# Kernel optimization log

Hardware: AMD Instinct MI355X
Metric: run time of the kernel (lower is better)

The kernel has to match this reference:

```python
import jax, jax.numpy as jnp
import numpy as np

D_MODEL = 1024
N_HEAD = 16
D_K = D_MODEL // N_HEAD
B, S = 2, 2048


def setup_inputs() -> dict:
    key = jax.random.key(0)
    ks = jax.random.split(key, 12)
    sc = 1.0 / np.sqrt(D_MODEL)
    return {
        "q": jax.random.normal(ks[0], (B, S, D_MODEL), jnp.float32),
        "k": jax.random.normal(ks[1], (B, S, D_MODEL), jnp.float32),
        "v": jax.random.normal(ks[2], (B, S, D_MODEL), jnp.float32),
        "mask": jax.random.randint(ks[3], (B, S, S), 0, 2, jnp.int32),
        # learned params (torch Linear convention: y = x @ W + b with W pre-transposed)
        "wq": jax.random.normal(ks[4], (D_MODEL, D_MODEL), jnp.float32) * sc,
        "bq": jax.random.normal(ks[5], (D_MODEL,), jnp.float32) * sc,
        "wk": jax.random.normal(ks[6], (D_MODEL, D_MODEL), jnp.float32) * sc,  # no bias
        "wv": jax.random.normal(ks[7], (D_MODEL, D_MODEL), jnp.float32) * sc,
        "bv": jax.random.normal(ks[8], (D_MODEL,), jnp.float32) * sc,
        "wf": jax.random.normal(ks[9], (D_MODEL, D_MODEL), jnp.float32) * sc,
        "bf": jax.random.normal(ks[10], (D_MODEL,), jnp.float32) * sc,
    }


def reference(q, k, v, mask, wq, bq, wk, wv, bv, wf, bf):
    bs = q.shape[0]
    temperature = jnp.asarray(D_K ** 0.5, q.dtype)
    # projections -> [b, h, s, d_k]
    qh = (q @ wq + bq).reshape(bs, -1, N_HEAD, D_K).transpose(0, 2, 1, 3)
    kh = (k @ wk).reshape(bs, -1, N_HEAD, D_K).transpose(0, 2, 1, 3)
    vh = (v @ wv + bv).reshape(bs, -1, N_HEAD, D_K).transpose(0, 2, 1, 3)
    # scores [b, h, sq, sk]
    attn = jnp.einsum("bhqd,bhkd->bhqk", qh, kh) / temperature
    m0 = (mask[:, None, :, :] == 0)  # mask==0 -> masked out, broadcast over heads
    attn = jnp.where(m0, -jnp.inf, attn)
    attn = jax.nn.softmax(attn, axis=-1)
    attn = jnp.where(m0, 0.0, attn)
    out = jnp.einsum("bhqk,bhkd->bhqd", attn, vh)
    out = out.transpose(0, 2, 1, 3).reshape(bs, -1, D_MODEL)
    return out @ wf + bf  # dropout is identity in eval mode
```

## Files before the change

kernel.cpp:

```cpp
#include <hip/hip_runtime.h>

#define D_MODEL 1024
#define NHEAD   16
#define DK      64
#define BATCH   2
#define SEQ     2048

typedef __attribute__((ext_vector_type(8))) short bf16x8;
typedef __attribute__((ext_vector_type(4))) short bf16x4;
typedef __attribute__((ext_vector_type(4))) float f32x4;
typedef __attribute__((ext_vector_type(2))) int i32x2;

#define QSCALE 0.18033688011f

__device__ __forceinline__ unsigned short f2b(float x) {
  unsigned u = __builtin_bit_cast(unsigned, x);
  u = (u + 0x7fffu + ((u >> 16) & 1u)) >> 16;
  return (unsigned short)u;
}
__device__ __forceinline__ unsigned short f2b_rhu(float x) {
  return (unsigned short)((__builtin_bit_cast(unsigned, x) + 0x8000u) >> 16);
}
__device__ __forceinline__ int pk2(float a, float b) {
  unsigned ua = __builtin_bit_cast(unsigned, a) + 0x8000u;
  unsigned ub = __builtin_bit_cast(unsigned, b) + 0x8000u;
  return (int)__builtin_amdgcn_perm(ub, ua, 0x07060302u);
}
__device__ __forceinline__ int pk2u(unsigned ua, unsigned ub) {
  return (int)__builtin_amdgcn_perm(ub + 0x8000u, ua + 0x8000u, 0x07060302u);
}

typedef const __attribute__((address_space(1))) void* gas_p;
typedef __attribute__((address_space(3))) void* las_p;
__device__ __forceinline__ void gll16(const void* g, void* l) {
  __builtin_amdgcn_global_load_lds((gas_p)g, (las_p)l, 16, 0, 0);
}

__device__ __forceinline__ f32x4 mfma16(bf16x4 a, bf16x4 b, f32x4 c) {
#if __has_builtin(__builtin_amdgcn_mfma_f32_16x16x16bf16_1k)
  return __builtin_amdgcn_mfma_f32_16x16x16bf16_1k(a, b, c, 0, 0, 0);
#else
  f32x4 d;
  asm("v_mfma_f32_16x16x16_bf16 %0, %1, %2, %3" : "=v"(d) : "v"(a), "v"(b), "v"(c));
  return d;
#endif
}

__global__ __launch_bounds__(256) void prep_kernel(
    const float* __restrict__ q, const float* __restrict__ k, const float* __restrict__ v,
    unsigned short* __restrict__ qb, unsigned short* __restrict__ kb,
    unsigned short* __restrict__ vb,
    const float* __restrict__ wq, const float* __restrict__ wk,
    const float* __restrict__ wv, const float* __restrict__ wf,
    unsigned short* __restrict__ wqt, unsigned short* __restrict__ wkt,
    unsigned short* __restrict__ wvt, unsigned short* __restrict__ wft,
    const int* __restrict__ mask, unsigned long long* __restrict__ mbits) {
  int bid = blockIdx.x, t = threadIdx.x;
  if (bid < 6144) {
    int by = bid >> 11, bx = bid & 2047;
    const float* src = by == 0 ? q : (by == 1 ? k : v);
    unsigned short* dst = by == 0 ? qb : (by == 1 ? kb : vb);
    size_t i = ((size_t)bx * 256 + t) * 8;
    float4 x0 = *(const float4*)&src[i];
    float4 x1 = *(const float4*)&src[i + 4];
    int4 w;
    w.x = pk2(x0.x, x0.y); w.y = pk2(x0.z, x0.w);
    w.z = pk2(x1.x, x1.y); w.w = pk2(x1.z, x1.w);
    *(int4*)&dst[i] = w;
  } else if (bid < 7168) {
    __shared__ float tile[64][65];
    int idx = bid - 6144;
    int bz = idx >> 8, by = (idx >> 4) & 15, bx = idx & 15;
    const float* w; unsigned short* wt;
    switch (bz) {
      case 0: w = wq; wt = wqt; break;
      case 1: w = wk; wt = wkt; break;
      case 2: w = wv; wt = wvt; break;
      default: w = wf; wt = wft; break;
    }
    int r0 = by * 64, c0 = bx * 64;
    for (int i = 0; i < 16; ++i) {
      int idx2 = t + i * 256; int r = idx2 >> 6, c = idx2 & 63;
      tile[r][c] = w[(size_t)(r0 + r) * D_MODEL + c0 + c];
    }
    __syncthreads();
    for (int i = 0; i < 16; ++i) {
      int idx2 = t + i * 256; int r = idx2 >> 6, c = idx2 & 63;
      wt[(size_t)(c0 + r) * D_MODEL + r0 + c] = f2b(tile[c][r]);
    }
  } else {
    int idx = bid - 7168;
    int lane = t & 63, wave = t >> 6;
    size_t base = ((size_t)idx * 4 + wave) * 256;
    unsigned long long b0 = __ballot(mask[base + lane] != 0);
    unsigned long long b1 = __ballot(mask[base + 64 + lane] != 0);
    unsigned long long b2 = __ballot(mask[base + 128 + lane] != 0);
    unsigned long long b3 = __ballot(mask[base + 192 + lane] != 0);
    if (lane == 0) {
      unsigned long long* p = &mbits[(size_t)idx * 16 + wave * 4];
      p[0] = b0; p[1] = b1; p[2] = b2; p[3] = b3;
    }
  }
}

__global__ __launch_bounds__(256) void gemm_qkv_kernel(
    const unsigned short* __restrict__ qb, const unsigned short* __restrict__ kb,
    const unsigned short* __restrict__ vb,
    const unsigned short* __restrict__ wqt, const unsigned short* __restrict__ wkt,
    const unsigned short* __restrict__ wvt,
    const float* __restrict__ bq, const float* __restrict__ bv,
    unsigned short* __restrict__ qh, unsigned short* __restrict__ kh,
    unsigned short* __restrict__ vt) {
  __shared__ unsigned short SB[16640];
  int bid = blockIdx.x;
  int xcd = bid & 7, slot = bid >> 3;
  int mi = slot & 3, zn = slot >> 2;
  int z = zn >> 3;
  int n0 = (zn & 7) * 128;
  int m0 = (mi * 8 + xcd) * 128;
  const unsigned short* A; const unsigned short* Bt;
  switch (z) {
    case 0:  A = qb; Bt = wqt; break;
    case 1:  A = kb; Bt = wkt; break;
    default: A = vb; Bt = wvt; break;
  }
  int t = threadIdx.x, lane = t & 63, wave = t >> 6;
  int l16 = lane & 15, quad = lane >> 4;
  int wm = (wave & 1) * 64, wn = (wave >> 1) * 64;
  f32x4 zero = {0.f, 0.f, 0.f, 0.f};
  f32x4 acc[4][4];
  for (int mt = 0; mt < 4; ++mt) for (int nt = 0; nt < 4; ++nt) acc[mt][nt] = zero;

  int drow = lane >> 2, dcol = (lane & 3) * 8;
  const unsigned short* asrc = A  + (size_t)(m0 + wave * 32 + drow) * D_MODEL + dcol;
  const unsigned short* bsrc = Bt + (size_t)(n0 + wave * 32 + drow) * D_MODEL + dcol;
  int dst = wave * 1024 + lane * 8;

#pragma unroll
  for (int g = 0; g < 2; ++g) {
    gll16(asrc + (size_t)(g * 16) * D_MODEL, &SB[dst + g * 512]);
    gll16(bsrc + (size_t)(g * 16) * D_MODEL, &SB[4096 + dst + g * 512]);
  }
  for (int it = 0; it < 32; ++it) {
    __syncthreads();
    if (it + 1 < 32) {
      int nb = ((it + 1) & 1) * 8192, kn = (it + 1) * 32;
#pragma unroll
      for (int g = 0; g < 2; ++g) {
        gll16(asrc + (size_t)(g * 16) * D_MODEL + kn, &SB[nb + dst + g * 512]);
        gll16(bsrc + (size_t)(g * 16) * D_MODEL + kn, &SB[nb + 4096 + dst + g * 512]);
      }
    }
    int cb = (it & 1) * 8192;
    bf16x8 a[4], b[4];
    for (int mt = 0; mt < 4; ++mt)
      a[mt] = *(const bf16x8*)&SB[cb + (wm + mt * 16 + l16) * 32 + quad * 8];
    for (int nt = 0; nt < 4; ++nt)
      b[nt] = *(const bf16x8*)&SB[cb + 4096 + (wn + nt * 16 + l16) * 32 + quad * 8];
    for (int mt = 0; mt < 4; ++mt)
      for (int nt = 0; nt < 4; ++nt)
        acc[mt][nt] = __builtin_amdgcn_mfma_f32_16x16x32_bf16(a[mt], b[nt], acc[mt][nt], 0, 0, 0);
  }

  if (z == 2) {
    __syncthreads();
#pragma unroll
    for (int nt = 0; nt < 4; ++nt) {
      int col = wn + nt * 16 + l16;
      float bb = bv[n0 + col];
      for (int mt = 0; mt < 4; ++mt)
        for (int r = 0; r < 4; ++r)
          SB[col * 130 + wm + mt * 16 + quad * 4 + r] = f2b_rhu(acc[mt][nt][r] + bb);
    }
    __syncthreads();
    int c = t >> 1, hf = t & 1;
    int colg = n0 + c, hh = colg >> 6, dd = colg & 63;
    int b_ = m0 >> 11, sbase = m0 & (SEQ - 1);
    unsigned short* dstp = vt + (((size_t)(b_ * NHEAD + hh)) * DK + dd) * SEQ + sbase + hf * 64;
#pragma unroll
    for (int j = 0; j < 8; ++j)
      *(int4*)(dstp + j * 8) = *(const int4*)&SB[c * 130 + hf * 64 + j * 8];
  } else {
    __syncthreads();
#pragma unroll
    for (int nt = 0; nt < 4; ++nt) {
      int lcol = wn + nt * 16 + l16;
      float bb = (z == 0) ? bq[n0 + lcol] : 0.f;
      for (int mt = 0; mt < 4; ++mt)
        for (int r = 0; r < 4; ++r) {
          float val = acc[mt][nt][r] + bb;
          if (z == 0) val *= QSCALE;
          SB[(wm + mt * 16 + quad * 4 + r) * 130 + lcol] = f2b_rhu(val);
        }
    }
    __syncthreads();
    unsigned short* outp = (z == 0) ? qh : kh;
    int b_ = m0 >> 11, sbase = m0 & (SEQ - 1);
    int h0 = n0 >> 6, c = t & 7;
#pragma unroll
    for (int pass = 0; pass < 8; ++pass) {
      int rp = pass * 32 + (t >> 3);
      int srow = rp >> 1, part = rp & 1;
      unsigned short* dstp = outp +
          (((size_t)(b_ * NHEAD + h0 + part)) * SEQ + sbase + srow) * DK + c * 8;
      *(int4*)dstp = *(const int4*)&SB[srow * 130 + part * 64 + c * 8];
    }
  }
}

__global__ __launch_bounds__(256) void gemm_out_kernel(
    const unsigned short* __restrict__ A, const unsigned short* __restrict__ Bt,
    const float* __restrict__ bias, float* __restrict__ out) {
  __shared__ unsigned short As[8192], Bs[8192];
  int bid = blockIdx.x;
  int xcd = bid & 7, slot = bid >> 3;
  int mi = slot & 7, n0 = (slot >> 3) * 64;
  int m0 = (mi * 8 + xcd) * 64;
  int t = threadIdx.x, lane = t & 63, wave = t >> 6;
  int l16 = lane & 15, quad = lane >> 4;
  int wm = (wave & 1) * 32, wn = (wave >> 1) * 32;
  f32x4 zero = {0.f, 0.f, 0.f, 0.f};
  f32x4 acc[2][2];
  for (int mt = 0; mt < 2; ++mt) for (int nt = 0; nt < 2; ++nt) acc[mt][nt] = zero;

  int drow = lane >> 2, dcol = (lane & 3) * 8;
  const unsigned short* asrc = A  + (size_t)(m0 + wave * 16 + drow) * D_MODEL + dcol;
  const unsigned short* bsrc = Bt + (size_t)(n0 + wave * 16 + drow) * D_MODEL + dcol;
  int dst = wave * 512 + lane * 8;

#pragma unroll
  for (int hf = 0; hf < 2; ++hf) {
    gll16(asrc + hf * 32, &As[dst + hf * 2048]);
    gll16(bsrc + hf * 32, &Bs[dst + hf * 2048]);
  }
  for (int it = 0; it < 16; ++it) {
    __syncthreads();
    if (it + 1 < 16) {
      int nb = ((it + 1) & 1) * 4096, kn = (it + 1) * 64;
#pragma unroll
      for (int hf = 0; hf < 2; ++hf) {
        gll16(asrc + kn + hf * 32, &As[nb + dst + hf * 2048]);
        gll16(bsrc + kn + hf * 32, &Bs[nb + dst + hf * 2048]);
      }
    }
    int cb = (it & 1) * 4096;
#pragma unroll
    for (int half = 0; half < 2; ++half) {
      bf16x8 a[2], b[2];
      for (int mt = 0; mt < 2; ++mt)
        a[mt] = *(const bf16x8*)&As[cb + half * 2048 + (wm + mt * 16 + l16) * 32 + quad * 8];
      for (int nt = 0; nt < 2; ++nt)
        b[nt] = *(const bf16x8*)&Bs[cb + half * 2048 + (wn + nt * 16 + l16) * 32 + quad * 8];
      for (int mt = 0; mt < 2; ++mt)
        for (int nt = 0; nt < 2; ++nt)
          acc[mt][nt] = __builtin_amdgcn_mfma_f32_16x16x32_bf16(a[mt], b[nt], acc[mt][nt], 0, 0, 0);
    }
  }
  for (int nt = 0; nt < 2; ++nt) {
    int col = n0 + wn + nt * 16 + l16;
    float bb = bias[col];
    for (int mt = 0; mt < 2; ++mt)
      for (int r = 0; r < 4; ++r) {
        int row = m0 + wm + mt * 16 + quad * 4 + r;
        out[(size_t)row * D_MODEL + col] = acc[mt][nt][r] + bb;
      }
  }
}

__global__ __launch_bounds__(512, 4) void attn_kernel(
    const unsigned short* __restrict__ qh, const unsigned short* __restrict__ kh,
    const unsigned short* __restrict__ vt, const unsigned long long* __restrict__ mbits,
    unsigned short* __restrict__ attb) {
  __shared__ unsigned short Ks[16384];
  __shared__ unsigned short Vs[16384];
  int bid = blockIdx.x;
  int xcd = bid & 7, slot = bid >> 3;
  int bh_ = 4 * xcd + (slot >> 4);
  int qt = slot & 15;
  int b = bh_ >> 4, h = bh_ & 15;
  int t = threadIdx.x, lane = t & 63, wave = t >> 6;
  int l16 = lane & 15, quad = lane >> 4;
  size_t bh = (size_t)b * NHEAD + h;

  const unsigned short* Kg = kh + bh * SEQ * DK;
  const unsigned short* Vg = vt + bh * DK * SEQ;
  const unsigned long long* mrow = mbits + (size_t)b * SEQ * (SEQ / 64);
  int qrowb = qt * 128 + wave * 16;

  bf16x8 qf[2];
  {
    const unsigned short* Qg = qh + (bh * SEQ + (size_t)(qrowb + l16)) * DK;
    qf[0] = *(const bf16x8*)&Qg[quad * 8];
    qf[1] = *(const bf16x8*)&Qg[32 + quad * 8];
  }

  int ksrow = t >> 3;
  int kschk = ((t & 7) ^ (ksrow & 7)) * 8;
  const unsigned short* ksrc = Kg + (size_t)ksrow * DK + kschk;
  int vsrow = t >> 4;
  int vschk = ((t & 15) ^ (vsrow & 15)) * 8;
  const unsigned short* vsrc = Vg + (size_t)vsrow * SEQ + vschk;
  int sdst = t * 8;

  int x7 = l16 & 7;
  int ka0 = l16 * 64 + ((quad ^ x7) * 8);
  int ka1 = l16 * 64 + (((4 + quad) ^ x7) * 8);
  int va[2][4];
#pragma unroll
  for (int sub = 0; sub < 2; ++sub)
#pragma unroll
    for (int nt = 0; nt < 4; ++nt)
      va[sub][nt] = l16 * 128 + (((sub * 8 + nt * 2 + (quad >> 1)) ^ l16) * 8)
                    + (quad & 1) * 4;

  size_t mi0 = (size_t)(qrowb + l16) * (SEQ / 64);

  bf16x4 ones4;
#pragma unroll
  for (int i = 0; i < 4; ++i) ones4[i] = (short)0x3F80;

  f32x4 zero = {0.f, 0.f, 0.f, 0.f};
  f32x4 accO[4], accRS = zero;
#pragma unroll
  for (int dt = 0; dt < 4; ++dt) accO[dt] = zero;

#pragma unroll
  for (int g = 0; g < 2; ++g) {
    gll16(ksrc + (size_t)(g * 64) * DK, &Ks[g * 4096 + sdst]);
    gll16(vsrc + (size_t)(g * 32) * SEQ, &Vs[g * 4096 + sdst]);
  }

  for (int tk = 0; tk < SEQ / 128; ++tk) {
    __syncthreads();
    if (tk + 1 < SEQ / 128) {
      int nb = ((tk + 1) & 1) * 8192;
      const unsigned short* kn = ksrc + (size_t)(tk + 1) * 128 * DK;
      const unsigned short* vn = vsrc + (tk + 1) * 128;
#pragma unroll
      for (int g = 0; g < 2; ++g) {
        gll16(kn + (size_t)(g * 64) * DK, &Ks[nb + g * 4096 + sdst]);
        gll16(vn + (size_t)(g * 32) * SEQ, &Vs[nb + g * 4096 + sdst]);
      }
    }
    unsigned long long mA0 = mrow[mi0 + 2 * tk];
    unsigned long long mA1 = mrow[mi0 + 2 * tk + 1];

    int cb = (tk & 1) * 8192;
#pragma unroll
    for (int sub = 0; sub < 2; ++sub) {
      int kb_ = cb + sub * 4096;
      f32x4 accS[4];
#pragma unroll
      for (int nt = 0; nt < 4; ++nt) accS[nt] = zero;
      __builtin_amdgcn_s_setprio(1);
#pragma unroll
      for (int step = 0; step < 2; ++step) {
        int ka = step ? ka1 : ka0;
#pragma unroll
        for (int nt = 0; nt < 4; ++nt) {
          bf16x8 kf = *(const bf16x8*)&Ks[kb_ + ka + nt * 1024];
          accS[nt] = __builtin_amdgcn_mfma_f32_16x16x32_bf16(kf, qf[step], accS[nt], 0, 0, 0);
        }
      }
      __builtin_amdgcn_s_setprio(0);

      unsigned long long mq = (sub ? mA1 : mA0) >> (quad * 4);
      unsigned mlo = (unsigned)mq, mhi = (unsigned)(mq >> 32);
      bf16x4 ap[4];
#pragma unroll
      for (int nt = 0; nt < 4; ++nt) {
        unsigned w = (nt < 2) ? mlo : mhi;
        unsigned pu[4];
#pragma unroll
        for (int r = 0; r < 4; ++r) {
          float pv = __builtin_amdgcn_exp2f(accS[nt][r]);
          int msk = ((int)(w << (31 - ((nt & 1) * 16 + r)))) >> 31;
          pu[r] = __builtin_bit_cast(unsigned, pv) & (unsigned)msk;
        }
        i32x2 wv;
        wv[0] = pk2u(pu[0], pu[1]);
        wv[1] = pk2u(pu[2], pu[3]);
        ap[nt] = __builtin_bit_cast(bf16x4, wv);
      }

      __builtin_amdgcn_s_setprio(1);
#pragma unroll
      for (int nt = 0; nt < 4; ++nt)
        accRS = mfma16(ap[nt], ones4, accRS);
#pragma unroll
      for (int nt = 0; nt < 4; ++nt) {
        int vb_ = cb + va[sub][nt];
#pragma unroll
        for (int dt = 0; dt < 4; ++dt) {
          bf16x4 vf = *(const bf16x4*)&Vs[vb_ + dt * 2048];
          accO[dt] = mfma16(ap[nt], vf, accO[dt]);
        }
      }
      __builtin_amdgcn_s_setprio(0);
    }
  }

#pragma unroll
  for (int r = 0; r < 4; ++r) {
    float sden = accRS[r];
    float inv = sden > 0.f ? 1.f / sden : 0.f;
    int row = qrowb + quad * 4 + r;
    size_t ob = ((size_t)b * SEQ + row) * D_MODEL + (size_t)h * DK;
    for (int dt = 0; dt < 4; ++dt)
      attb[ob + dt * 16 + l16] = f2b_rhu(accO[dt][r] * inv);
  }
}

extern "C" void kernel_launch(void* const* d_in, const int* in_sizes, int n_in,
                              void* d_out, int out_size, void* d_ws, size_t ws_size,
                              hipStream_t stream) {
  (void)in_sizes; (void)n_in; (void)out_size; (void)ws_size;
  const float* q    = (const float*)d_in[0];
  const float* k    = (const float*)d_in[1];
  const float* v    = (const float*)d_in[2];
  const int*   mask = (const int*)d_in[3];
  const float* wq   = (const float*)d_in[4];
  const float* bq   = (const float*)d_in[5];
  const float* wk   = (const float*)d_in[6];
  const float* wv   = (const float*)d_in[7];
  const float* bv   = (const float*)d_in[8];
  const float* wf   = (const float*)d_in[9];
  const float* bf   = (const float*)d_in[10];

  char* ws = (char*)d_ws;
  unsigned short* wft  = (unsigned short*)(ws + 0);
  unsigned short* wqt  = (unsigned short*)(ws + 2097152);
  unsigned short* wkt  = (unsigned short*)(ws + 4194304);
  unsigned short* wvt  = (unsigned short*)(ws + 6291456);
  unsigned short* attb = (unsigned short*)(ws + 2097152);
  unsigned short* qhp  = (unsigned short*)(ws + 10485760);
  unsigned short* khp  = (unsigned short*)(ws + 18874368);
  unsigned short* vtp  = (unsigned short*)(ws + 27262976);
  unsigned long long* mbits = (unsigned long long*)(ws + 35651584);
  unsigned short* vb   = (unsigned short*)(ws + 36700160);
  unsigned short* qb   = (unsigned short*)d_out;
  unsigned short* kb   = (unsigned short*)d_out + 4194304;

  hipLaunchKernelGGL(prep_kernel, dim3(15360), dim3(256), 0, stream,
                     q, k, v, qb, kb, vb,
                     wq, wk, wv, wf, wqt, wkt, wvt, wft, mask, mbits);
  hipLaunchKernelGGL(gemm_qkv_kernel, dim3(768), dim3(256), 0, stream,
                     qb, kb, vb, wqt, wkt, wvt, bq, bv, qhp, khp, vtp);
  hipLaunchKernelGGL(attn_kernel, dim3(512), dim3(512), 0, stream,
                     qhp, khp, vtp, mbits, attb);
  hipLaunchKernelGGL(gemm_out_kernel, dim3(1024), dim3(256), 0, stream,
                     attb, wft, bf, (float*)d_out);
}
```

Baseline: 250.1 us.

## Switch attention kernel to 32x32x16 MFMA tiles with 4 waves per block

Rewrites the attention inner loop to use 32x32x16 bf16 MFMA instead of 16x16 variants, so each wave now handles 32 query rows. Blocks shrink from 512 to 256 threads. The V-transpose stage in the QKV GEMM permutes row order so the V layout in shared memory matches the new P-fragment layout. The aim is fewer MFMA issues and fewer LDS reads per unit of work, at the cost of more accumulator registers and fewer waves for latency hiding.

```diff
diff --git a/kernel.cpp b/kernel.cpp
--- a/kernel.cpp
+++ b/kernel.cpp
@@ -7,9 +7,9 @@
 #define SEQ     2048
 
 typedef __attribute__((ext_vector_type(8))) short bf16x8;
-typedef __attribute__((ext_vector_type(4))) short bf16x4;
 typedef __attribute__((ext_vector_type(4))) float f32x4;
-typedef __attribute__((ext_vector_type(2))) int i32x2;
+typedef __attribute__((ext_vector_type(16))) float f32x16;
+typedef __attribute__((ext_vector_type(4))) int i32x4;
 
 #define QSCALE 0.18033688011f
 
@@ -36,14 +36,8 @@
   __builtin_amdgcn_global_load_lds((gas_p)g, (las_p)l, 16, 0, 0);
 }
 
-__device__ __forceinline__ f32x4 mfma16(bf16x4 a, bf16x4 b, f32x4 c) {
-#if __has_builtin(__builtin_amdgcn_mfma_f32_16x16x16bf16_1k)
-  return __builtin_amdgcn_mfma_f32_16x16x16bf16_1k(a, b, c, 0, 0, 0);
-#else
-  f32x4 d;
-  asm("v_mfma_f32_16x16x16_bf16 %0, %1, %2, %3" : "=v"(d) : "v"(a), "v"(b), "v"(c));
-  return d;
-#endif
+__device__ __forceinline__ f32x16 mfma32(bf16x8 a, bf16x8 b, f32x16 c) {
+  return __builtin_amdgcn_mfma_f32_32x32x16_bf16(a, b, c, 0, 0, 0);
 }
 
 __global__ __launch_bounds__(256) void prep_kernel(
@@ -164,13 +158,14 @@
 
   if (z == 2) {
     __syncthreads();
+    int qs = ((quad & 1) << 1) | (quad >> 1);
 #pragma unroll
     for (int nt = 0; nt < 4; ++nt) {
       int col = wn + nt * 16 + l16;
       float bb = bv[n0 + col];
       for (int mt = 0; mt < 4; ++mt)
         for (int r = 0; r < 4; ++r)
-          SB[col * 130 + wm + mt * 16 + quad * 4 + r] = f2b_rhu(acc[mt][nt][r] + bb);
+          SB[col * 130 + wm + mt * 16 + qs * 4 + r] = f2b_rhu(acc[mt][nt][r] + bb);
     }
     __syncthreads();
     int c = t >> 1, hf = t & 1;
@@ -267,7 +262,7 @@
   }
 }
 
-__global__ __launch_bounds__(512, 4) void attn_kernel(
+__global__ __launch_bounds__(256, 2) void attn_kernel(
     const unsigned short* __restrict__ qh, const unsigned short* __restrict__ kh,
     const unsigned short* __restrict__ vt, const unsigned long long* __restrict__ mbits,
     unsigned short* __restrict__ attb) {
@@ -279,19 +274,20 @@
   int qt = slot & 15;
   int b = bh_ >> 4, h = bh_ & 15;
   int t = threadIdx.x, lane = t & 63, wave = t >> 6;
-  int l16 = lane & 15, quad = lane >> 4;
+  int l32 = lane & 31, hi = lane >> 5;
   size_t bh = (size_t)b * NHEAD + h;
 
   const unsigned short* Kg = kh + bh * SEQ * DK;
   const unsigned short* Vg = vt + bh * DK * SEQ;
   const unsigned long long* mrow = mbits + (size_t)b * SEQ * (SEQ / 64);
-  int qrowb = qt * 128 + wave * 16;
-
-  bf16x8 qf[2];
+  int qrowb = qt * 128 + wave * 32;
+
+  bf16x8 qf[4];
   {
-    const unsigned short* Qg = qh + (bh * SEQ + (size_t)(qrowb + l16)) * DK;
-    qf[0] = *(const bf16x8*)&Qg[quad * 8];
-    qf[1] = *(const bf16x8*)&Qg[32 + quad * 8];
+    const unsigned short* Qg = qh + (bh * SEQ + (size_t)(qrowb + l32)) * DK;
+#pragma unroll
+    for (int step = 0; step < 4; ++step)
+      qf[step] = *(const bf16x8*)&Qg[(step * 2 + hi) * 8];
   }
 
   int ksrow = t >> 3;
@@ -302,32 +298,28 @@
   const unsigned short* vsrc = Vg + (size_t)vsrow * SEQ + vschk;
   int sdst = t * 8;
 
-  int x7 = l16 & 7;
-  int ka0 = l16 * 64 + ((quad ^ x7) * 8);
-  int ka1 = l16 * 64 + (((4 + quad) ^ x7) * 8);
-  int va[2][4];
-#pragma unroll
-  for (int sub = 0; sub < 2; ++sub)
-#pragma unroll
-    for (int nt = 0; nt < 4; ++nt)
-      va[sub][nt] = l16 * 128 + (((sub * 8 + nt * 2 + (quad >> 1)) ^ l16) * 8)
-                    + (quad & 1) * 4;
-
-  size_t mi0 = (size_t)(qrowb + l16) * (SEQ / 64);
-
-  bf16x4 ones4;
-#pragma unroll
-  for (int i = 0; i < 4; ++i) ones4[i] = (short)0x3F80;
-
-  f32x4 zero = {0.f, 0.f, 0.f, 0.f};
-  f32x4 accO[4], accRS = zero;
-#pragma unroll
-  for (int dt = 0; dt < 4; ++dt) accO[dt] = zero;
-
-#pragma unroll
-  for (int g = 0; g < 2; ++g) {
-    gll16(ksrc + (size_t)(g * 64) * DK, &Ks[g * 4096 + sdst]);
-    gll16(vsrc + (size_t)(g * 32) * SEQ, &Vs[g * 4096 + sdst]);
+  int kx = l32 & 7;
+  int kaddr[4];
+#pragma unroll
+  for (int step = 0; step < 4; ++step)
+    kaddr[step] = l32 * 64 + (((step * 2 + hi) ^ kx) * 8);
+  int vx = l32 & 15;
+
+  size_t mi0 = (size_t)(qrowb + l32) * (SEQ / 64);
+
+  bf16x8 ones8;
+#pragma unroll
+  for (int i = 0; i < 8; ++i) ones8[i] = (short)0x3F80;
+
+  f32x16 zero16;
+#pragma unroll
+  for (int i = 0; i < 16; ++i) zero16[i] = 0.f;
+  f32x16 accO0 = zero16, accO1 = zero16, accRS = zero16;
+
+#pragma unroll
+  for (int g = 0; g < 4; ++g) {
+    gll16(ksrc + (size_t)(g * 32) * DK, &Ks[g * 2048 + sdst]);
+    gll16(vsrc + (size_t)(g * 16) * SEQ, &Vs[g * 2048 + sdst]);
   }
 
   for (int tk = 0; tk < SEQ / 128; ++tk) {
@@ -337,77 +329,71 @@
       const unsigned short* kn = ksrc + (size_t)(tk + 1) * 128 * DK;
       const unsigned short* vn = vsrc + (tk + 1) * 128;
 #pragma unroll
-      for (int g = 0; g < 2; ++g) {
-        gll16(kn + (size_t)(g * 64) * DK, &Ks[nb + g * 4096 + sdst]);
-        gll16(vn + (size_t)(g * 32) * SEQ, &Vs[nb + g * 4096 + sdst]);
-      }
-    }
-    unsigned long long mA0 = mrow[mi0 + 2 * tk];
-    unsigned long long mA1 = mrow[mi0 + 2 * tk + 1];
+      for (int g = 0; g < 4; ++g) {
+        gll16(kn + (size_t)(g * 32) * DK, &Ks[nb + g * 2048 + sdst]);
+        gll16(vn + (size_t)(g * 16) * SEQ, &Vs[nb + g * 2048 + sdst]);
+      }
+    }
+    unsigned long long m0 = mrow[mi0 + 2 * tk];
+    unsigned long long m1 = mrow[mi0 + 2 * tk + 1];
 
     int cb = (tk & 1) * 8192;
 #pragma unroll
-    for (int sub = 0; sub < 2; ++sub) {
-      int kb_ = cb + sub * 4096;
-      f32x4 accS[4];
-#pragma unroll
-      for (int nt = 0; nt < 4; ++nt) accS[nt] = zero;
+    for (int kt = 0; kt < 4; ++kt) {
+      f32x16 accS = zero16;
       __builtin_amdgcn_s_setprio(1);
 #pragma unroll
-      for (int step = 0; step < 2; ++step) {
-        int ka = step ? ka1 : ka0;
-#pragma unroll
-        for (int nt = 0; nt < 4; ++nt) {
-          bf16x8 kf = *(const bf16x8*)&Ks[kb_ + ka + nt * 1024];
-          accS[nt] = __builtin_amdgcn_mfma_f32_16x16x32_bf16(kf, qf[step], accS[nt], 0, 0, 0);
-        }
+      for (int step = 0; step < 4; ++step) {
+        bf16x8 kf = *(const bf16x8*)&Ks[cb + kt * 2048 + kaddr[step]];
+        accS = mfma32(kf, qf[step], accS);
       }
       __builtin_amdgcn_s_setprio(0);
 
-      unsigned long long mq = (sub ? mA1 : mA0) >> (quad * 4);
-      unsigned mlo = (unsigned)mq, mhi = (unsigned)(mq >> 32);
-      bf16x4 ap[4];
-#pragma unroll
-      for (int nt = 0; nt < 4; ++nt) {
-        unsigned w = (nt < 2) ? mlo : mhi;
-        unsigned pu[4];
-#pragma unroll
-        for (int r = 0; r < 4; ++r) {
-          float pv = __builtin_amdgcn_exp2f(accS[nt][r]);
-          int msk = ((int)(w << (31 - ((nt & 1) * 16 + r)))) >> 31;
-          pu[r] = __builtin_bit_cast(unsigned, pv) & (unsigned)msk;
-        }
-        i32x2 wv;
-        wv[0] = pk2u(pu[0], pu[1]);
-        wv[1] = pk2u(pu[2], pu[3]);
-        ap[nt] = __builtin_bit_cast(bf16x4, wv);
-      }
+      unsigned wk_ = (unsigned)(((kt < 2) ? m0 : m1) >> ((kt & 1) * 32));
+      unsigned w = wk_ >> (4 * hi);
+      unsigned pu[16];
+#pragma unroll
+      for (int r = 0; r < 16; ++r) {
+        float pv = __builtin_amdgcn_exp2f(accS[r]);
+        const int pos = (r & 3) + 8 * (r >> 2);
+        int msk = ((int)(w << (31 - pos))) >> 31;
+        pu[r] = __builtin_bit_cast(unsigned, pv) & (unsigned)msk;
+      }
+      i32x4 w0v = {pk2u(pu[0], pu[1]),  pk2u(pu[2], pu[3]),
+                   pk2u(pu[4], pu[5]),  pk2u(pu[6], pu[7])};
+      i32x4 w1v = {pk2u(pu[8], pu[9]),  pk2u(pu[10], pu[11]),
+                   pk2u(pu[12], pu[13]), pk2u(pu[14], pu[15])};
+      bf16x8 ap0 = __builtin_bit_cast(bf16x8, w0v);
+      bf16x8 ap1 = __builtin_bit_cast(bf16x8, w1v);
 
       __builtin_amdgcn_s_setprio(1);
-#pragma unroll
-      for (int nt = 0; nt < 4; ++nt)
-        accRS = mfma16(ap[nt], ones4, accRS);
-#pragma unroll
-      for (int nt = 0; nt < 4; ++nt) {
-        int vb_ = cb + va[sub][nt];
-#pragma unroll
-        for (int dt = 0; dt < 4; ++dt) {
-          bf16x4 vf = *(const bf16x4*)&Vs[vb_ + dt * 2048];
-          accO[dt] = mfma16(ap[nt], vf, accO[dt]);
-        }
+      accRS = mfma32(ap0, ones8, accRS);
+      accRS = mfma32(ap1, ones8, accRS);
+      {
+        int c0 = ((kt * 4 + hi) ^ vx) * 8;
+        int c1 = ((kt * 4 + 2 + hi) ^ vx) * 8;
+        bf16x8 vf00 = *(const bf16x8*)&Vs[cb + l32 * 128 + c0];
+        bf16x8 vf01 = *(const bf16x8*)&Vs[cb + 4096 + l32 * 128 + c0];
+        bf16x8 vf10 = *(const bf16x8*)&Vs[cb + l32 * 128 + c1];
+        bf16x8 vf11 = *(const bf16x8*)&Vs[cb + 4096 + l32 * 128 + c1];
+        accO0 = mfma32(ap0, vf00, accO0);
+        accO1 = mfma32(ap0, vf01, accO1);
+        accO0 = mfma32(ap1, vf10, accO0);
+        accO1 = mfma32(ap1, vf11, accO1);
       }
       __builtin_amdgcn_s_setprio(0);
     }
   }
 
 #pragma unroll
-  for (int r = 0; r < 4; ++r) {
+  for (int r = 0; r < 16; ++r) {
     float sden = accRS[r];
     float inv = sden > 0.f ? 1.f / sden : 0.f;
-    int row = qrowb + quad * 4 + r;
-    size_t ob = ((size_t)b * SEQ + row) * D_MODEL + (size_t)h * DK;
-    for (int dt = 0; dt < 4; ++dt)
-      attb[ob + dt * 16 + l16] = f2b_rhu(accO[dt][r] * inv);
+    int qq = (r & 3) + 8 * (r >> 2) + 4 * hi;
+    int row = qrowb + qq;
+    size_t ob = ((size_t)b * SEQ + row) * D_MODEL + (size_t)h * DK + l32;
+    attb[ob] = f2b_rhu(accO0[r] * inv);
+    attb[ob + 32] = f2b_rhu(accO1[r] * inv);
   }
 }
 
@@ -446,7 +432,7 @@
                      wq, wk, wv, wf, wqt, wkt, wvt, wft, mask, mbits);
   hipLaunchKernelGGL(gemm_qkv_kernel, dim3(768), dim3(256), 0, stream,
                      qb, kb, vb, wqt, wkt, wvt, bq, bv, qhp, khp, vtp);
-  hipLaunchKernelGGL(attn_kernel, dim3(512), dim3(512), 0, stream,
+  hipLaunchKernelGGL(attn_kernel, dim3(512), dim3(256), 0, stream,
                      qhp, khp, vtp, mbits, attb);
   hipLaunchKernelGGL(gemm_out_kernel, dim3(1024), dim3(256), 0, stream,
                      attb, wft, bf, (float*)d_out);
```

Measured after the change: 255.9 us. 2.3% more time.
